# Kernel tuning notes

Hardware: AMD Instinct MI355X
Metric: run time of the kernel (lower is better)

## Reference

```python
import jax, jax.numpy as jnp
import numpy as np

B, S, HID = 1, 2048, 4096
H, NOPE, ROPE, VD = 32, 128, 64, 128
QKD = NOPE + ROPE
Q_RANK, KV_RANK = 1536, 512
IDX_H, IDX_D, TOPK = 16, 128, 1024
EPS, THETA = 1e-5, 10000.0


def rmsnorm(x, w):
    return x * jax.lax.rsqrt(jnp.mean(x * x, axis=-1, keepdims=True) + EPS) * w


def rope_interleaved(x, pos):
    # x: [..., s, d]; rope_interleave=True -> rotate adjacent pairs
    d = x.shape[-1]
    inv_freq = 1.0 / (THETA ** (jnp.arange(0, d, 2, dtype=jnp.float32) / d))
    ang = pos[:, None] * inv_freq[None, :]  # [s, d/2]
    cos, sin = jnp.cos(ang), jnp.sin(ang)
    x2 = x.reshape(*x.shape[:-1], d // 2, 2)
    x0, x1 = x2[..., 0], x2[..., 1]
    return jnp.stack([x0 * cos - x1 * sin, x1 * cos + x0 * sin], axis=-1).reshape(x.shape)


def setup_inputs() -> dict:
    key = jax.random.key(0)
    ks = jax.random.split(key, 12)
    s = 0.02
    return {
        'hidden_states': jax.random.normal(ks[0], (B, S, HID), jnp.float32),
        'q_a_w': jax.random.normal(ks[1], (HID, Q_RANK), jnp.float32) * s,
        'q_a_norm_w': jnp.ones((Q_RANK,), jnp.float32),
        'q_b_w': jax.random.normal(ks[2], (Q_RANK, H * QKD), jnp.float32) * s,
        'kv_a_w': jax.random.normal(ks[3], (HID, KV_RANK + ROPE), jnp.float32) * s,
        'kv_a_norm_w': jnp.ones((KV_RANK,), jnp.float32),
        'kv_b_w': jax.random.normal(ks[4], (KV_RANK, H * (NOPE + VD)), jnp.float32) * s,
        'o_w': jax.random.normal(ks[5], (H * VD, HID), jnp.float32) * s,
        'idx_wq_w': jax.random.normal(ks[6], (HID, IDX_H * IDX_D), jnp.float32) * s,
        'idx_wk_w': jax.random.normal(ks[7], (HID, IDX_D), jnp.float32) * s,
        'idx_weights_w': jax.random.normal(ks[8], (HID, IDX_H), jnp.float32) * s,
    }


def reference(hidden_states, q_a_w, q_a_norm_w, q_b_w, kv_a_w, kv_a_norm_w,
              kv_b_w, o_w, idx_wq_w, idx_wk_w, idx_weights_w):
    b, s, _ = hidden_states.shape
    pos = jnp.arange(s, dtype=jnp.float32)

    # ---- MLA latent projections ----
    q_lat = rmsnorm(hidden_states @ q_a_w, q_a_norm_w)                 # [b,s,Q_RANK]
    q = (q_lat @ q_b_w).reshape(b, s, H, QKD).transpose(0, 2, 1, 3)    # [b,h,s,qkd]
    q_nope, q_pe = q[..., :NOPE], q[..., NOPE:]

    ckv = hidden_states @ kv_a_w                                       # [b,s,KV_RANK+ROPE]
    kv_lat, k_pe = ckv[..., :KV_RANK], ckv[..., KV_RANK:]
    kv = (rmsnorm(kv_lat, kv_a_norm_w) @ kv_b_w).reshape(b, s, H, NOPE + VD).transpose(0, 2, 1, 3)
    k_nope, v = kv[..., :NOPE], kv[..., NOPE:]

    q_pe = rope_interleaved(q_pe, pos)
    k_pe = rope_interleaved(k_pe[:, None, :, :], pos)                  # [b,1,s,ROPE] shared MQA rope head

    scores = (jnp.einsum('bhqd,bhkd->bhqk', q_nope, k_nope)
              + jnp.einsum('bhqd,bhkd->bhqk', q_pe, k_pe)) * (QKD ** -0.5)

    # ---- DSA lightning indexer: per-query top-k key selection ----
    iq = (hidden_states @ idx_wq_w).reshape(b, s, IDX_H, IDX_D)
    ik = hidden_states @ idx_wk_w                                      # [b,s,IDX_D]
    iw = (hidden_states @ idx_weights_w) * (IDX_H ** -0.5)             # [b,s,IDX_H]
    idx_scores = jnp.einsum('bqn,bnqk->bqk', iw,
                            jax.nn.relu(jnp.einsum('bqnd,bkd->bnqk', iq, ik))) * (IDX_D ** -0.5)
    causal = pos[:, None] >= pos[None, :]                              # [s,s]
    idx_scores = jnp.where(causal, idx_scores, -jnp.inf)
    _, topk_idx = jax.lax.top_k(idx_scores, TOPK)                      # [b,s,TOPK]
    bi = jnp.arange(b)[:, None, None]
    qi = jnp.arange(s)[None, :, None]
    topk_mask = jnp.zeros((b, s, s), bool).at[bi, qi, topk_idx].set(True)
    mask = topk_mask & causal                                          # [b,s,s]

    scores = jnp.where(mask[:, None], scores, -jnp.inf)
    attn = jax.nn.softmax(scores, axis=-1)
    out = jnp.einsum('bhqk,bhkd->bqhd', attn, v).reshape(b, s, H * VD)
    return out @ o_w
```

## Files before the change

### kernel.cpp

```cpp
#include <hip/hip_runtime.h>
#include <math.h>

#define S_LEN 2048
#define HIDDEN 4096
#define NHEAD 32
#define D_NOPE 128
#define D_ROPE 64
#define D_V 128
#define D_QK 192
#define QRANK 1536
#define KVRANK 512
#define IDXH 16
#define IDXD 128
#define KSEL 1024
#define NIDX 2304

typedef __attribute__((ext_vector_type(8))) short bf16x8;
typedef __attribute__((ext_vector_type(4))) float f32x4;
typedef __attribute__((ext_vector_type(4))) unsigned short u16x4;

__device__ __forceinline__ unsigned short f2b(float f) {
    union { float f; unsigned int u; } x; x.f = f;
    unsigned int r = x.u + 0x7FFFu + ((x.u >> 16) & 1u);
    return (unsigned short)(r >> 16);
}
__device__ __forceinline__ float b2f(unsigned short u) {
    union { unsigned int u; float f; } x; x.u = ((unsigned int)u) << 16; return x.f;
}

__device__ __forceinline__ void gload16(const void* g, const void* l) {
    __builtin_amdgcn_global_load_lds(
        (const __attribute__((address_space(1))) unsigned int*)(unsigned long long)g,
        (__attribute__((address_space(3))) unsigned int*)(unsigned int)(unsigned long long)l,
        16, 0, 0);
}

template <int OUT_BF16>
__global__ __launch_bounds__(256) void gemm_bf16(const unsigned short* __restrict__ A,
                                                 const unsigned short* __restrict__ Bt,
                                                 void* __restrict__ Cv,
                                                 int K, int ldc, float alpha) {
    __shared__ __align__(16) unsigned char lds[32768];
    const int tid = threadIdx.x;
    const int w = tid >> 6, lane = tid & 63;
    const int lr = lane & 15, g = lane >> 4;
    const int gx = gridDim.x;
    const int nwg = gx * gridDim.y;
    const int flat = blockIdx.y * gx + blockIdx.x;
    const int swz = (flat & 7) * (nwg >> 3) + (flat >> 3);
    const int bm = (swz / gx) * 128, bn = (swz % gx) * 128;
    const int wm = (w >> 1) * 64, wn = (w & 1) * 64;

    f32x4 acc[4][4];
#pragma unroll
    for (int i = 0; i < 4; ++i)
#pragma unroll
        for (int j = 0; j < 4; ++j) acc[i][j] = (f32x4){0.f, 0.f, 0.f, 0.f};

    int a_off[2], b_off[2];
#pragma unroll
    for (int issue = 0; issue < 2; ++issue) {
        const int off = issue * 4096 + w * 1024 + lane * 16;
        const int row = off >> 6, slot = (off >> 4) & 3;
        a_off[issue] = (bm + row) * K + ((slot ^ (row & 3)) << 3);
        b_off[issue] = (bn + row) * K + ((slot ^ (row & 3)) << 3);
    }

    const int KT = K >> 5;
    auto stage = [&](int t, int buf) {
        const int k0 = t << 5;
        unsigned char* l = lds + buf * 16384;
        gload16(A + a_off[0] + k0, l + w * 1024);
        gload16(A + a_off[1] + k0, l + 4096 + w * 1024);
        gload16(Bt + b_off[0] + k0, l + 8192 + w * 1024);
        gload16(Bt + b_off[1] + k0, l + 8192 + 4096 + w * 1024);
    };

    stage(0, 0);
    for (int t = 0; t < KT; ++t) {
        if (t + 1 < KT) {
            stage(t + 1, (t + 1) & 1);
            asm volatile("s_waitcnt vmcnt(4)" ::: "memory");
        } else {
            asm volatile("s_waitcnt vmcnt(0)" ::: "memory");
        }
        __syncthreads();
        const unsigned char* l = lds + (t & 1) * 16384;

        bf16x8 af[4], bfr[4];
#pragma unroll
        for (int i = 0; i < 4; ++i) {
            const int rowA = wm + i * 16 + lr;
            af[i] = *(const bf16x8*)(l + rowA * 64 + ((g ^ (rowA & 3)) << 4));
            const int rowB = wn + i * 16 + lr;
            bfr[i] = *(const bf16x8*)(l + 8192 + rowB * 64 + ((g ^ (rowB & 3)) << 4));
        }
#pragma unroll
        for (int i = 0; i < 4; ++i)
#pragma unroll
            for (int j = 0; j < 4; ++j)
                acc[i][j] = __builtin_amdgcn_mfma_f32_16x16x32_bf16(af[i], bfr[j], acc[i][j], 0, 0, 0);
        __syncthreads();
    }

#pragma unroll
    for (int i = 0; i < 4; ++i) {
        const int m = bm + wm + i * 16 + g * 4;
#pragma unroll
        for (int j = 0; j < 4; ++j) {
            const int n = bn + wn + j * 16 + lr;
            if (OUT_BF16) {
                unsigned short* Cb = (unsigned short*)Cv;
#pragma unroll
                for (int r = 0; r < 4; ++r)
                    Cb[(size_t)(m + r) * ldc + n] = f2b(acc[i][j][r] * alpha);
            } else {
                float* Cf = (float*)Cv;
#pragma unroll
                for (int r = 0; r < 4; ++r)
                    Cf[(size_t)(m + r) * ldc + n] = acc[i][j][r] * alpha;
            }
        }
    }
}

__global__ __launch_bounds__(256) void gemm_split(const unsigned short* __restrict__ Ah,
                                                  const unsigned short* __restrict__ Al,
                                                  const unsigned short* __restrict__ Bh,
                                                  const unsigned short* __restrict__ Bl,
                                                  float* __restrict__ C0,
                                                  float* __restrict__ C1) {
    const int K = HIDDEN, ldc = NIDX;
    const int bid = blockIdx.x;
    const int wf = (bid & 7) * 38 + (bid >> 3);
    const int kz = (wf >= 152) ? 1 : 0;
    const int wgid = wf - kz * 152;
    int x, y;
    if (wgid < 144) { y = 8 + wgid / 18; x = wgid % 18; }
    else            { x = 16; y = wgid - 144; }
    const int bm = y * 128, bn = x * 128;
    float* __restrict__ C = kz ? C1 : C0;

    __shared__ __align__(16) unsigned char lds[65536];
    const int tid = threadIdx.x;
    const int w = tid >> 6, lane = tid & 63;
    const int lr = lane & 15, g = lane >> 4;
    const int wm = (w >> 1) * 64, wn = (w & 1) * 64;

    f32x4 acc[4][4];
#pragma unroll
    for (int i = 0; i < 4; ++i)
#pragma unroll
        for (int j = 0; j < 4; ++j) acc[i][j] = (f32x4){0.f, 0.f, 0.f, 0.f};

    int a_off[2], b_off[2];
#pragma unroll
    for (int issue = 0; issue < 2; ++issue) {
        const int off = issue * 4096 + w * 1024 + lane * 16;
        const int row = off >> 6, slot = (off >> 4) & 3;
        a_off[issue] = (bm + row) * K + ((slot ^ (row & 3)) << 3) + kz * 2048;
        b_off[issue] = (bn + row) * K + ((slot ^ (row & 3)) << 3) + kz * 2048;
    }

    const int KT = 2048 >> 5;
    auto stage = [&](int t, int buf) {
        const int k0 = t << 5;
        unsigned char* l = lds + buf * 32768;
        gload16(Ah + a_off[0] + k0, l + w * 1024);
        gload16(Ah + a_off[1] + k0, l + 4096 + w * 1024);
        gload16(Al + a_off[0] + k0, l + 8192 + w * 1024);
        gload16(Al + a_off[1] + k0, l + 8192 + 4096 + w * 1024);
        gload16(Bh + b_off[0] + k0, l + 16384 + w * 1024);
        gload16(Bh + b_off[1] + k0, l + 16384 + 4096 + w * 1024);
        gload16(Bl + b_off[0] + k0, l + 24576 + w * 1024);
        gload16(Bl + b_off[1] + k0, l + 24576 + 4096 + w * 1024);
    };

    stage(0, 0);
    for (int t = 0; t < KT; ++t) {
        if (t + 1 < KT) {
            stage(t + 1, (t + 1) & 1);
            asm volatile("s_waitcnt vmcnt(8)" ::: "memory");
        } else {
            asm volatile("s_waitcnt vmcnt(0)" ::: "memory");
        }
        __syncthreads();
        const unsigned char* l = lds + (t & 1) * 32768;

        bf16x8 afh[4], afl[4], bfh[4], bfl[4];
#pragma unroll
        for (int i = 0; i < 4; ++i) {
            const int rowA = wm + i * 16 + lr;
            const int offA = rowA * 64 + ((g ^ (rowA & 3)) << 4);
            afh[i] = *(const bf16x8*)(l + offA);
            afl[i] = *(const bf16x8*)(l + 8192 + offA);
            const int rowB = wn + i * 16 + lr;
            const int offB = rowB * 64 + ((g ^ (rowB & 3)) << 4);
            bfh[i] = *(const bf16x8*)(l + 16384 + offB);
            bfl[i] = *(const bf16x8*)(l + 24576 + offB);
        }
#pragma unroll
        for (int i = 0; i < 4; ++i)
#pragma unroll
            for (int j = 0; j < 4; ++j) {
                acc[i][j] = __builtin_amdgcn_mfma_f32_16x16x32_bf16(afh[i], bfh[j], acc[i][j], 0, 0, 0);
                acc[i][j] = __builtin_amdgcn_mfma_f32_16x16x32_bf16(afh[i], bfl[j], acc[i][j], 0, 0, 0);
                acc[i][j] = __builtin_amdgcn_mfma_f32_16x16x32_bf16(afl[i], bfh[j], acc[i][j], 0, 0, 0);
            }
        __syncthreads();
    }

#pragma unroll
    for (int i = 0; i < 4; ++i) {
        const int m = bm + wm + i * 16 + g * 4;
#pragma unroll
        for (int j = 0; j < 4; ++j) {
            const int n = bn + wn + j * 16 + lr;
#pragma unroll
            for (int r = 0; r < 4; ++r)
                C[(size_t)(m + r) * ldc + n] = acc[i][j][r];
        }
    }
}

__global__ __launch_bounds__(256) void conv_split_h(const float* __restrict__ src,
                                                    unsigned short* __restrict__ dhi,
                                                    unsigned short* __restrict__ dlo) {
    const int i = blockIdx.x * 256 + threadIdx.x;
    const float4 v = ((const float4*)src)[i];
    u16x4 hi, lo;
    const float xs[4] = {v.x, v.y, v.z, v.w};
#pragma unroll
    for (int j = 0; j < 4; ++j) {
        const unsigned short h = f2b(xs[j]);
        hi[j] = h;
        lo[j] = f2b(xs[j] - b2f(h));
    }
    *(u16x4*)(dhi + (size_t)i * 4) = hi;
    *(u16x4*)(dlo + (size_t)i * 4) = lo;
}

__global__ __launch_bounds__(256) void conv_split_iq(const float* __restrict__ C0,
                                                     const float* __restrict__ C1,
                                                     unsigned short* __restrict__ iqh,
                                                     unsigned short* __restrict__ iql,
                                                     unsigned short* __restrict__ ikh,
                                                     unsigned short* __restrict__ ikl,
                                                     float* __restrict__ iwbuf) {
    const int i = blockIdx.x * 256 + threadIdx.x;
    const int row = i / 548, c4 = (i - row * 548) * 4;
    const float4 v0 = *(const float4*)(C0 + (size_t)row * NIDX + c4);
    const float4 v1 = *(const float4*)(C1 + (size_t)row * NIDX + c4);
    const float xs[4] = {v0.x + v1.x, v0.y + v1.y, v0.z + v1.z, v0.w + v1.w};
    if (c4 >= 2176) {
        *(float4*)(iwbuf + (size_t)row * 16 + (c4 - 2176)) =
            (float4){xs[0], xs[1], xs[2], xs[3]};
        return;
    }
    u16x4 hi, lo;
#pragma unroll
    for (int j = 0; j < 4; ++j) {
        const unsigned short h = f2b(xs[j]);
        hi[j] = h;
        lo[j] = f2b(xs[j] - b2f(h));
    }
    if (c4 < 2048) {
        *(u16x4*)(iqh + (size_t)row * 2048 + c4) = hi;
        *(u16x4*)(iql + (size_t)row * 2048 + c4) = lo;
    } else {
        *(u16x4*)(ikh + (size_t)row * 128 + c4 - 2048) = hi;
        *(u16x4*)(ikl + (size_t)row * 128 + c4 - 2048) = lo;
    }
}

__global__ __launch_bounds__(256) void wtrans(const float* __restrict__ W,
                                              unsigned short* __restrict__ Bt,
                                              int K, int Nsrc) {
    const int n0 = blockIdx.x * 64, k0 = blockIdx.y * 64;
    __shared__ unsigned short lv[64][72];
    const int tid = threadIdx.x;
#pragma unroll
    for (int it = 0; it < 16; ++it) {
        const int idx = tid + it * 256;
        const int kr = idx >> 6, n = idx & 63;
        const float v = (n0 + n < Nsrc) ? W[(size_t)(k0 + kr) * Nsrc + n0 + n] : 0.f;
        lv[n][kr] = f2b(v);
    }
    __syncthreads();
#pragma unroll
    for (int it = 0; it < 16; ++it) {
        const int idx = tid + it * 256;
        const int n = idx >> 6, kk = idx & 63;
        Bt[(size_t)(n0 + n) * K + k0 + kk] = lv[n][kk];
    }
}

__global__ __launch_bounds__(256) void wtrans_split(const float* __restrict__ W,
                                                    unsigned short* __restrict__ Bth,
                                                    unsigned short* __restrict__ Btl,
                                                    int K, int Nsrc) {
    const int n0 = blockIdx.x * 64, k0 = blockIdx.y * 64;
    __shared__ float lv[64][65];
    const int tid = threadIdx.x;
#pragma unroll
    for (int it = 0; it < 16; ++it) {
        const int idx = tid + it * 256;
        const int kr = idx >> 6, n = idx & 63;
        lv[n][kr] = (n0 + n < Nsrc) ? W[(size_t)(k0 + kr) * Nsrc + n0 + n] : 0.f;
    }
    __syncthreads();
#pragma unroll
    for (int it = 0; it < 16; ++it) {
        const int idx = tid + it * 256;
        const int n = idx >> 6, kk = idx & 63;
        const float x = lv[n][kk];
        const unsigned short h = f2b(x);
        Bth[(size_t)(n0 + n) * K + k0 + kk] = h;
        Btl[(size_t)(n0 + n) * K + k0 + kk] = f2b(x - b2f(h));
    }
}

__global__ __launch_bounds__(256) void rmsnormb(const float* __restrict__ in,
                                                const float* __restrict__ w,
                                                unsigned short* __restrict__ out,
                                                int W, int in_stride) {
    const int row = blockIdx.x;
    const int tid = threadIdx.x;
    const float* x = in + (size_t)row * in_stride;
    float ss = 0.f;
    for (int i = tid; i < W; i += 256) {
        float v = x[i];
        ss += v * v;
    }
    __shared__ float red[256];
    red[tid] = ss;
    __syncthreads();
    for (int s = 128; s > 0; s >>= 1) {
        if (tid < s) red[tid] += red[tid + s];
        __syncthreads();
    }
    const float scale = rsqrtf(red[0] / (float)W + 1e-5f);
    for (int i = tid; i < W; i += 256) out[(size_t)row * W + i] = f2b(x[i] * scale * w[i]);
}

__global__ __launch_bounds__(256) void rope_q16(unsigned short* __restrict__ q) {
    const int idx = blockIdx.x * 256 + threadIdx.x;
    if (idx >= S_LEN * NHEAD * (D_ROPE / 2)) return;
    const int i = idx & 31;
    const int h = (idx >> 5) & 31;
    const int s = idx >> 10;
    const float inv = __expf(-(float)i * (logf(10000.f) / 32.f));
    const float ang = (float)s * inv;
    const float cs = cosf(ang), sn = sinf(ang);
    unsigned short* p = q + (size_t)s * (NHEAD * D_QK) + h * D_QK + D_NOPE + 2 * i;
    const float x0 = b2f(p[0]), x1 = b2f(p[1]);
    p[0] = f2b(x0 * cs - x1 * sn);
    p[1] = f2b(x1 * cs + x0 * sn);
}

__global__ __launch_bounds__(256) void rope_k16(const float* __restrict__ C1,
                                                unsigned short* __restrict__ kpe16) {
    const int idx = blockIdx.x * 256 + threadIdx.x;
    if (idx >= S_LEN * (D_ROPE / 2)) return;
    const int i = idx & 31;
    const int s = idx >> 5;
    const float inv = __expf(-(float)i * (logf(10000.f) / 32.f));
    const float ang = (float)s * inv;
    const float cs = cosf(ang), sn = sinf(ang);
    const float* p = C1 + (size_t)s * 2176 + 2048 + 2 * i;
    const float x0 = p[0], x1 = p[1];
    kpe16[(size_t)s * D_ROPE + 2 * i] = f2b(x0 * cs - x1 * sn);
    kpe16[(size_t)s * D_ROPE + 2 * i + 1] = f2b(x1 * cs + x0 * sn);
}

#define ISC_IKH 0
#define ISC_IKL 16384
#define ISC_IQH 32768
#define ISC_IQL 49152
#define ISC_IW 65536

__global__ __launch_bounds__(256) void idx_score_mfma(const unsigned short* __restrict__ iqh,
                                                      const unsigned short* __restrict__ iql,
                                                      const unsigned short* __restrict__ ikh,
                                                      const unsigned short* __restrict__ ikl,
                                                      const float* __restrict__ iwbuf,
                                                      float* __restrict__ iscore) {
    const int kt = blockIdx.x, qt = blockIdx.y + 16;
    if (kt > qt) return;
    const int q0 = qt * 64, k0 = kt * 64;
    __shared__ __align__(16) unsigned char smem[69632];
    const int tid = threadIdx.x;
    const int w = tid >> 6, lane = tid & 63;
    const int g = lane >> 4, lr = lane & 15;

#pragma unroll
    for (int it = 0; it < 4; ++it) {
        const int j = tid + it * 256;
        const int row = j >> 4, slot = j & 15;
        const int dst = row * 256 + ((slot ^ (row & 7)) << 4);
        *(uint4*)(smem + ISC_IKH + dst) = *(const uint4*)(ikh + (size_t)(k0 + row) * 128 + slot * 8);
        *(uint4*)(smem + ISC_IKL + dst) = *(const uint4*)(ikl + (size_t)(k0 + row) * 128 + slot * 8);
    }
    {
        const int r = tid >> 2, c4 = (tid & 3) * 4;
        const float4 v = *(const float4*)(iwbuf + (size_t)(q0 + r) * 16 + c4);
        float4 sv = {v.x * 0.25f, v.y * 0.25f, v.z * 0.25f, v.w * 0.25f};
        *(float4*)(smem + ISC_IW + r * 64 + c4 * 4) = sv;
    }

    f32x4 tot[4];
#pragma unroll
    for (int j = 0; j < 4; ++j) tot[j] = (f32x4){0.f, 0.f, 0.f, 0.f};

    for (int n = 0; n < IDXH; ++n) {
        __syncthreads();
#pragma unroll
        for (int it = 0; it < 4; ++it) {
            const int j = tid + it * 256;
            const int row = j >> 4, slot = j & 15;
            const int dst = row * 256 + ((slot ^ (row & 7)) << 4);
            *(uint4*)(smem + ISC_IQH + dst) =
                *(const uint4*)(iqh + (size_t)(q0 + row) * 2048 + n * 128 + slot * 8);
            *(uint4*)(smem + ISC_IQL + dst) =
                *(const uint4*)(iql + (size_t)(q0 + row) * 2048 + n * 128 + slot * 8);
        }
        __syncthreads();

        bf16x8 aH[4], aL[4];
        const int ar = w * 16 + lr;
#pragma unroll
        for (int kk = 0; kk < 4; ++kk) {
            const int off = ar * 256 + (((kk * 4 + g) ^ (ar & 7)) << 4);
            aH[kk] = *(const bf16x8*)(smem + ISC_IQH + off);
            aL[kk] = *(const bf16x8*)(smem + ISC_IQL + off);
        }
        float wv[4];
#pragma unroll
        for (int r = 0; r < 4; ++r)
            wv[r] = *(const float*)(smem + ISC_IW + (w * 16 + g * 4 + r) * 64 + n * 4);

#pragma unroll
        for (int jj = 0; jj < 4; ++jj) {
            f32x4 s = (f32x4){0.f, 0.f, 0.f, 0.f};
#pragma unroll
            for (int kk = 0; kk < 4; ++kk) {
                const int br = jj * 16 + lr;
                const int off = br * 256 + (((kk * 4 + g) ^ (br & 7)) << 4);
                const bf16x8 bH = *(const bf16x8*)(smem + ISC_IKH + off);
                const bf16x8 bL = *(const bf16x8*)(smem + ISC_IKL + off);
                s = __builtin_amdgcn_mfma_f32_16x16x32_bf16(aH[kk], bH, s, 0, 0, 0);
                s = __builtin_amdgcn_mfma_f32_16x16x32_bf16(aH[kk], bL, s, 0, 0, 0);
                s = __builtin_amdgcn_mfma_f32_16x16x32_bf16(aL[kk], bH, s, 0, 0, 0);
            }
#pragma unroll
            for (int r = 0; r < 4; ++r) tot[jj][r] += wv[r] * fmaxf(s[r], 0.f);
        }
    }

    const float sc = 0.08838834764831845f;
#pragma unroll
    for (int jj = 0; jj < 4; ++jj)
#pragma unroll
        for (int r = 0; r < 4; ++r)
            iscore[(size_t)(q0 + w * 16 + g * 4 + r) * S_LEN + k0 + jj * 16 + lr] =
                tot[jj][r] * sc;
}

__global__ __launch_bounds__(256) void topk_kernel(const float* __restrict__ iscore,
                                                   unsigned char* __restrict__ maskb) {
    const int q = blockIdx.x;
    const int tid = threadIdx.x;
    const int nk = q + 1;
    unsigned char* mrow = maskb + (size_t)q * 256;
    if (nk <= KSEL) {
        unsigned char b = 0;
#pragma unroll
        for (int bi = 0; bi < 8; ++bi)
            if (tid * 8 + bi <= q) b |= (unsigned char)(1 << bi);
        mrow[tid] = b;
        return;
    }
    __shared__ unsigned int uv[S_LEN];
    __shared__ unsigned int hist[256];
    __shared__ unsigned int sh_pfx, sh_rem;
    const float* srow = iscore + (size_t)q * S_LEN;
    for (int k = tid; k < nk; k += 256) {
        unsigned int b = __float_as_uint(srow[k]);
        uv[k] = (b & 0x80000000u) ? ~b : (b | 0x80000000u);
    }
    if (tid == 0) { sh_pfx = 0u; sh_rem = KSEL; }
    __syncthreads();

    const int lane = tid & 63;
#pragma unroll
    for (int shift = 24; shift >= 0; shift -= 8) {
        const unsigned int pfx = sh_pfx;
        const unsigned int rem = sh_rem;
        const unsigned int pmask = (shift == 24) ? 0u : (0xFFFFFFFFu << (shift + 8));
        hist[tid] = 0u;
        __syncthreads();
        for (int k = tid; k < nk; k += 256) {
            const unsigned int u = uv[k];
            if ((u & pmask) == pfx)
                atomicAdd(&hist[(u >> shift) & 255u], 1u);
        }
        __syncthreads();
        const unsigned int h0 = hist[lane * 4], h1 = hist[lane * 4 + 1];
        const unsigned int h2 = hist[lane * 4 + 2], h3 = hist[lane * 4 + 3];
        unsigned int sufp = h0 + h1 + h2 + h3;
#pragma unroll
        for (int off = 1; off < 64; off <<= 1) {
            const unsigned int o = __shfl_down(sufp, off);
            if (lane + off < 64) sufp += o;
        }
        unsigned int run = __shfl_down(sufp, 1);
        if (lane == 63) run = 0u;
        const unsigned int s3 = run + h3;
        const unsigned int s2 = s3 + h2;
        const unsigned int s1 = s2 + h1;
        const unsigned int s0 = s1 + h0;
        int bsel = -1;
        unsigned int gt = 0u;
        if (s3 >= rem && run < rem)      { bsel = 3; gt = run; }
        else if (s2 >= rem && s3 < rem)  { bsel = 2; gt = s3; }
        else if (s1 >= rem && s2 < rem)  { bsel = 1; gt = s2; }
        else if (s0 >= rem && s1 < rem)  { bsel = 0; gt = s1; }
        if (bsel >= 0) {
            sh_pfx = pfx | ((unsigned int)(lane * 4 + bsel) << shift);
            sh_rem = rem - gt;
        }
        __syncthreads();
    }
    const unsigned int T = sh_pfx;
    const int r = (int)sh_rem;
    unsigned char b = 0;
#pragma unroll
    for (int bi = 0; bi < 8; ++bi) {
        const int k = tid * 8 + bi;
        if (k < nk) {
            const unsigned int u = uv[k];
            if (u > T) {
                b |= (unsigned char)(1 << bi);
            } else if (u == T) {
                int rank = 0;
                for (int j = 0; j < k; ++j) rank += (uv[j] == T) ? 1 : 0;
                if (rank < r) b |= (unsigned char)(1 << bi);
            }
        }
    }
    mrow[tid] = b;
}

__global__ __launch_bounds__(256) void pack_k16(const unsigned short* __restrict__ kv16,
                                                const unsigned short* __restrict__ kpe16,
                                                unsigned short* __restrict__ kb16) {
    const int idx = blockIdx.x * 256 + threadIdx.x;
    const int h = idx / (S_LEN * D_QK);
    const int rem = idx - h * (S_LEN * D_QK);
    const int s = rem / D_QK;
    const int d = rem - s * D_QK;
    kb16[idx] = (d < 128) ? kv16[(size_t)s * 8192 + h * 256 + d]
                          : kpe16[(size_t)s * D_ROPE + (d - 128)];
}

__global__ __launch_bounds__(256) void pack_vT16(const unsigned short* __restrict__ kv16,
                                                 unsigned short* __restrict__ vT) {
    const int st = blockIdx.x, h = blockIdx.y;
    const int s0 = st * 64;
    __shared__ unsigned short lv[64][130];
    const int tid = threadIdx.x;
#pragma unroll
    for (int it = 0; it < 32; ++it) {
        const int idx = tid + it * 256;
        const int sl = idx >> 7, d = idx & 127;
        lv[sl][d] = kv16[(size_t)(s0 + sl) * 8192 + h * 256 + 128 + d];
    }
    __syncthreads();
#pragma unroll
    for (int it = 0; it < 32; ++it) {
        const int idx = tid + it * 256;
        const int d = idx >> 6, sl = idx & 63;
        vT[(size_t)(h * 128 + d) * S_LEN + s0 + sl] = lv[sl][d];
    }
}

#define KVB 64
#define AQB 128
#define AT_K0 0
#define AT_K1 24576
#define AT_V0 49152
#define AT_V1 65536
#define AT_P 81920
#define AT_M 100352
#define AT_TOT 133120

__global__ __launch_bounds__(512) void attn_mfma_kernel(
    const unsigned short* __restrict__ qbuf16,
    const unsigned short* __restrict__ kb16,
    const unsigned short* __restrict__ vT,
    const unsigned char* __restrict__ maskb,
    unsigned short* __restrict__ ab16) {
    __shared__ __align__(16) unsigned char smem[AT_TOT];
    const int bid = blockIdx.x;
    const int xcd = bid & 7, jj = bid >> 3;
    const int h = (xcd << 2) | (jj & 3);
    const int qt = 15 - (jj >> 2);
    const int q0 = qt * AQB;
    const int tid = threadIdx.x;
    const int w = tid >> 6, lane = tid & 63;
    const int g = lane >> 4, lr = lane & 15;
    const int wub = (tid & ~63) * 16;

    const unsigned char* kbase = (const unsigned char*)(kb16 + (size_t)h * S_LEN * D_QK);
    const unsigned char* vbase = (const unsigned char*)(vT + (size_t)h * 128 * S_LEN);
    const unsigned char* mbase = maskb + (size_t)q0 * 256;

    bf16x8 qf[6];
    {
        const unsigned short* qrow =
            qbuf16 + (size_t)(q0 + w * 16 + lr) * (NHEAD * D_QK) + h * D_QK;
#pragma unroll
        for (int c = 0; c < 6; ++c) qf[c] = *(const bf16x8*)(qrow + c * 32 + g * 8);
    }

#pragma unroll
    for (int it = 0; it < 4; ++it) {
        const int j = tid + it * 512;
        gload16(mbase + (size_t)j * 16, smem + AT_M + it * 8192 + wub);
    }

    auto stageK = [&](int k0, int kb) {
#pragma unroll
        for (int it = 0; it < 3; ++it) {
            const int j = tid + it * 512;
            const int row = j / 24, cs = j - row * 24;
            const int scs = (cs & ~7) | ((cs & 7) ^ (row & 7));
            gload16(kbase + (size_t)(k0 + row) * 384 + scs * 16, smem + kb + it * 8192 + wub);
        }
    };
    auto stageV = [&](int k0, int vb) {
#pragma unroll
        for (int it = 0; it < 2; ++it) {
            const int j = tid + it * 512;
            const int d = j >> 3, sl = j & 7;
            gload16(vbase + ((size_t)d * S_LEN + k0) * 2 + ((sl ^ (d & 7)) * 16),
                    smem + vb + it * 8192 + wub);
        }
    };

    f32x4 O[8];
#pragma unroll
    for (int db = 0; db < 8; ++db) O[db] = (f32x4){0.f, 0.f, 0.f, 0.f};
    float mS[4] = {-INFINITY, -INFINITY, -INFINITY, -INFINITY};
    float lS[4] = {0.f, 0.f, 0.f, 0.f};
    unsigned short* Pw = (unsigned short*)(smem + AT_P + w * 2304);

    const int nt = 2 * qt + 2;
    stageK(0, AT_K0);
    stageV(0, AT_V0);
    asm volatile("s_waitcnt vmcnt(0)" ::: "memory");
    __syncthreads();

    for (int t = 0; t < nt; ++t) {
        const int cK = AT_K0 + (t & 1) * 24576;
        const int cV = AT_V0 + (t & 1) * 16384;
        if (t + 1 < nt) {
            stageK((t + 1) * KVB, AT_K0 + ((t + 1) & 1) * 24576);
            stageV((t + 1) * KVB, AT_V0 + ((t + 1) & 1) * 16384);
        }

        f32x4 a[4];
#pragma unroll
        for (int j = 0; j < 4; ++j) a[j] = (f32x4){0.f, 0.f, 0.f, 0.f};
        __builtin_amdgcn_s_setprio(1);
#pragma unroll
        for (int c = 0; c < 6; ++c) {
            const int s = c * 4 + g;
#pragma unroll
            for (int j = 0; j < 4; ++j) {
                const int row = j * 16 + lr;
                const int scs = (s & ~7) | ((s & 7) ^ (lr & 7));
                const bf16x8 b = *(const bf16x8*)(smem + cK + row * 384 + scs * 16);
                a[j] = __builtin_amdgcn_mfma_f32_16x16x32_bf16(qf[c], b, a[j], 0, 0, 0);
            }
        }
        __builtin_amdgcn_s_setprio(0);

        const int moff = (t * KVB) >> 3;
        float corr[4];
#pragma unroll
        for (int r = 0; r < 4; ++r) {
            const int qrl = w * 16 + g * 4 + r;
            const unsigned int mlo = *(const unsigned int*)(smem + AT_M + qrl * 256 + moff);
            const unsigned int mhi = *(const unsigned int*)(smem + AT_M + qrl * 256 + moff + 4);
            float sv[4];
            sv[0] = ((mlo >> lr) & 1u) ? a[0][r] : -INFINITY;
            sv[1] = ((mlo >> (lr + 16)) & 1u) ? a[1][r] : -INFINITY;
            sv[2] = ((mhi >> lr) & 1u) ? a[2][r] : -INFINITY;
            sv[3] = ((mhi >> (lr + 16)) & 1u) ? a[3][r] : -INFINITY;
            float tm = fmaxf(fmaxf(sv[0], sv[1]), fmaxf(sv[2], sv[3]));
            tm = fmaxf(tm, __shfl_xor(tm, 1));
            tm = fmaxf(tm, __shfl_xor(tm, 2));
            tm = fmaxf(tm, __shfl_xor(tm, 4));
            tm = fmaxf(tm, __shfl_xor(tm, 8));
            const float mn = fmaxf(mS[r], tm);
            const float co = (mS[r] > -INFINITY) ? __expf(mS[r] - mn) : 0.f;
            float p[4];
#pragma unroll
            for (int j = 0; j < 4; ++j) p[j] = (sv[j] > -INFINITY) ? __expf(sv[j] - mn) : 0.f;
            float rs = (p[0] + p[1]) + (p[2] + p[3]);
            rs += __shfl_xor(rs, 1);
            rs += __shfl_xor(rs, 2);
            rs += __shfl_xor(rs, 4);
            rs += __shfl_xor(rs, 8);
            lS[r] = lS[r] * co + rs;
            mS[r] = mn;
            corr[r] = co;
#pragma unroll
            for (int j = 0; j < 4; ++j) Pw[(g * 4 + r) * 72 + j * 16 + lr] = f2b(p[j]);
        }
#pragma unroll
        for (int db = 0; db < 8; ++db) {
            O[db][0] *= corr[0];
            O[db][1] *= corr[1];
            O[db][2] *= corr[2];
            O[db][3] *= corr[3];
        }

        asm volatile("s_waitcnt lgkmcnt(0)" ::: "memory");
        __builtin_amdgcn_sched_barrier(0);

        __builtin_amdgcn_s_setprio(1);
#pragma unroll
        for (int c2 = 0; c2 < 2; ++c2) {
            const bf16x8 pA = *(const bf16x8*)((const unsigned char*)Pw + lr * 144 + c2 * 64 + g * 16);
#pragma unroll
            for (int db = 0; db < 8; ++db) {
                const int d = db * 16 + lr;
                const int s2 = c2 * 4 + g;
                const bf16x8 bV = *(const bf16x8*)(smem + cV + d * 128 + ((s2 ^ (d & 7)) << 4));
                O[db] = __builtin_amdgcn_mfma_f32_16x16x32_bf16(pA, bV, O[db], 0, 0, 0);
            }
        }
        __builtin_amdgcn_s_setprio(0);

        asm volatile("s_waitcnt vmcnt(0)" ::: "memory");
        __syncthreads();
    }

#pragma unroll
    for (int r = 0; r < 4; ++r) {
        const float inv = (lS[r] > 0.f) ? 1.f / lS[r] : 0.f;
        const int qg = q0 + w * 16 + g * 4 + r;
        unsigned short* orow = ab16 + (size_t)qg * (NHEAD * D_V) + h * D_V;
#pragma unroll
        for (int db = 0; db < 8; ++db) orow[db * 16 + lr] = f2b(O[db][r] * inv);
    }
}

extern "C" void kernel_launch(void* const* d_in, const int* in_sizes, int n_in,
                              void* d_out, int out_size, void* d_ws, size_t ws_size,
                              hipStream_t stream) {
    const float* hidden        = (const float*)d_in[0];
    const float* q_a_w         = (const float*)d_in[1];
    const float* q_a_norm_w    = (const float*)d_in[2];
    const float* q_b_w         = (const float*)d_in[3];
    const float* kv_a_w        = (const float*)d_in[4];
    const float* kv_a_norm_w   = (const float*)d_in[5];
    const float* kv_b_w        = (const float*)d_in[6];
    const float* o_w           = (const float*)d_in[7];
    const float* idx_wq_w      = (const float*)d_in[8];
    const float* idx_wk_w      = (const float*)d_in[9];
    const float* idx_weights_w = (const float*)d_in[10];
    float* out = (float*)d_out;

    char* ws = (char*)d_ws;
    unsigned short* BtAll = (unsigned short*)(ws + 0);
    unsigned short* kv16  = (unsigned short*)(ws + 0);
    unsigned short* owT   = (unsigned short*)(ws + 0);
    unsigned short* h16    = (unsigned short*)(ws + 33554432);
    unsigned short* h_lo   = (unsigned short*)(ws + 50331648);
    unsigned short* qbuf16 = (unsigned short*)(ws + 33554432);
    float* C1          = (float*)(ws + 67108864);
    unsigned short* vT = (unsigned short*)(ws + 67108864);
    unsigned short* BtIdxH = (unsigned short*)(ws + 84934656);
    unsigned short* BtIdxL = (unsigned short*)(ws + 103809024);
    unsigned short* kb16   = (unsigned short*)(ws + 84934656);
    float* Cidx         = (float*)(ws + 122683392);
    unsigned short* qbT = (unsigned short*)(ws + 122683392);
    unsigned short* iqh  = (unsigned short*)(ws + 141557760);
    unsigned short* iql  = (unsigned short*)(ws + 149946368);
    unsigned short* ikh  = (unsigned short*)(ws + 158334976);
    unsigned short* ikl  = (unsigned short*)(ws + 158859264);
    unsigned short* kvbT = (unsigned short*)(ws + 141557760);
    float* iscr          = (float*)(ws + 159383552);
    unsigned short* ab16 = (unsigned short*)(ws + 159383552);
    unsigned char* maskb  = (unsigned char*)(ws + 176160768);
    unsigned short* qa16  = (unsigned short*)(ws + 180355072);
    unsigned short* kvn16 = (unsigned short*)(ws + 186646528);
    unsigned short* kpe16 = (unsigned short*)(ws + 188743680);
    float* iwbuf = (float*)(ws + 189005824);
    float* Cidx2 = (float*)(ws + 189136896);
    (void)ws_size; (void)in_sizes; (void)n_in; (void)out_size;

    const dim3 blk(256);
    const float QK_SCALE = 0.07216878364870323f;

    conv_split_h<<<8192, blk, 0, stream>>>(hidden, h16, h_lo);

    wtrans<<<dim3(24, 64), blk, 0, stream>>>(q_a_w, BtAll, HIDDEN, QRANK);
    wtrans<<<dim3(9, 64), blk, 0, stream>>>(kv_a_w, BtAll + (size_t)1536 * HIDDEN, HIDDEN, KVRANK + D_ROPE);
    wtrans<<<dim3(1, 64), blk, 0, stream>>>(q_a_w, BtAll + (size_t)2112 * HIDDEN, HIDDEN, 0);
    gemm_bf16<0><<<dim3(17, 16), blk, 0, stream>>>(h16, BtAll, C1, HIDDEN, 2176, 1.f);

    rmsnormb<<<S_LEN, blk, 0, stream>>>(C1, q_a_norm_w, qa16, QRANK, 2176);
    rmsnormb<<<S_LEN, blk, 0, stream>>>(C1 + 1536, kv_a_norm_w, kvn16, KVRANK, 2176);
    rope_k16<<<(S_LEN * 32 + 255) / 256, blk, 0, stream>>>(C1, kpe16);

    wtrans_split<<<dim3(32, 64), blk, 0, stream>>>(idx_wq_w, BtIdxH, BtIdxL, HIDDEN, IDXH * IDXD);
    wtrans_split<<<dim3(2, 64), blk, 0, stream>>>(idx_wk_w, BtIdxH + (size_t)2048 * HIDDEN,
                                                  BtIdxL + (size_t)2048 * HIDDEN, HIDDEN, IDXD);
    wtrans_split<<<dim3(2, 64), blk, 0, stream>>>(idx_weights_w, BtIdxH + (size_t)2176 * HIDDEN,
                                                  BtIdxL + (size_t)2176 * HIDDEN, HIDDEN, IDXH);
    gemm_split<<<dim3(304), blk, 0, stream>>>(h16, h_lo, BtIdxH, BtIdxL, Cidx, Cidx2);
    conv_split_iq<<<4384, blk, 0, stream>>>(Cidx, Cidx2, iqh, iql, ikh, ikl, iwbuf);
    idx_score_mfma<<<dim3(32, 16), blk, 0, stream>>>(iqh, iql, ikh, ikl, iwbuf, iscr);
    topk_kernel<<<S_LEN, blk, 0, stream>>>(iscr, maskb);

    wtrans<<<dim3(96, 24), blk, 0, stream>>>(q_b_w, qbT, QRANK, NHEAD * D_QK);
    wtrans<<<dim3(128, 8), blk, 0, stream>>>(kv_b_w, kvbT, KVRANK, NHEAD * 256);
    gemm_bf16<1><<<dim3(48, 16), blk, 0, stream>>>(qa16, qbT, qbuf16, QRANK, NHEAD * D_QK, QK_SCALE);
    gemm_bf16<1><<<dim3(64, 16), blk, 0, stream>>>(kvn16, kvbT, kv16, KVRANK, NHEAD * 256, 1.f);
    rope_q16<<<(S_LEN * NHEAD * 32 + 255) / 256, blk, 0, stream>>>(qbuf16);

    pack_k16<<<(NHEAD * S_LEN * D_QK) / 256, blk, 0, stream>>>(kv16, kpe16, kb16);
    pack_vT16<<<dim3(S_LEN / 64, NHEAD), blk, 0, stream>>>(kv16, vT);
    attn_mfma_kernel<<<dim3(512), dim3(512), 0, stream>>>(qbuf16, kb16, vT, maskb, ab16);

    wtrans<<<dim3(64, 64), blk, 0, stream>>>(o_w, owT, NHEAD * D_V, HIDDEN);
    gemm_bf16<0><<<dim3(32, 16), blk, 0, stream>>>(ab16, owT, out, NHEAD * D_V, HIDDEN, 1.f);
}
```

Measured before the change: 773.0 us.

## Fuse kv_b GEMM epilogue into K/V^T packing and slim attention LDS usage

Adds a dedicated kv_b GEMM whose epilogue writes the K-nope part directly into the per-head packed K buffer and transposes V tiles through LDS straight into vT. Rope for k_pe is broadcast straight into each head's slot of the packed K buffer. This removes the intermediate kv16/kpe16 buffers and the pack_k16/pack_vT16 kernels. The attention kernel now loads mask bits into registers per tile instead of staging the whole mask in LDS, and reuses the current K buffer for P behind an extra barrier. Together these shrink LDS from about 130KB to 80KB, and O rescaling is skipped when the correction factor is exactly 1. The costs are an added barrier per tile, more scattered global mask reads and strided K stores from the GEMM epilogue.

```diff
diff --git a/kernel.cpp b/kernel.cpp
--- a/kernel.cpp
+++ b/kernel.cpp
@@ -121,6 +121,109 @@
                     Cf[(size_t)(m + r) * ldc + n] = acc[i][j][r] * alpha;
             }
         }
+    }
+}
+
+__global__ __launch_bounds__(256) void gemm_kvb(const unsigned short* __restrict__ A,
+                                                const unsigned short* __restrict__ Bt,
+                                                unsigned short* __restrict__ kb16,
+                                                unsigned short* __restrict__ vT) {
+    __shared__ __align__(16) unsigned char lds[34816];
+    const int tid = threadIdx.x;
+    const int w = tid >> 6, lane = tid & 63;
+    const int lr = lane & 15, g = lane >> 4;
+    const int gx = gridDim.x;
+    const int nwg = gx * gridDim.y;
+    const int flat = blockIdx.y * gx + blockIdx.x;
+    const int swz = (flat & 7) * (nwg >> 3) + (flat >> 3);
+    const int bm = (swz / gx) * 128, bn = (swz % gx) * 128;
+    const int wm = (w >> 1) * 64, wn = (w & 1) * 64;
+    const int K = KVRANK;
+
+    f32x4 acc[4][4];
+#pragma unroll
+    for (int i = 0; i < 4; ++i)
+#pragma unroll
+        for (int j = 0; j < 4; ++j) acc[i][j] = (f32x4){0.f, 0.f, 0.f, 0.f};
+
+    int a_off[2], b_off[2];
+#pragma unroll
+    for (int issue = 0; issue < 2; ++issue) {
+        const int off = issue * 4096 + w * 1024 + lane * 16;
+        const int row = off >> 6, slot = (off >> 4) & 3;
+        a_off[issue] = (bm + row) * K + ((slot ^ (row & 3)) << 3);
+        b_off[issue] = (bn + row) * K + ((slot ^ (row & 3)) << 3);
+    }
+
+    const int KT = K >> 5;
+    auto stage = [&](int t, int buf) {
+        const int k0 = t << 5;
+        unsigned char* l = lds + buf * 16384;
+        gload16(A + a_off[0] + k0, l + w * 1024);
+        gload16(A + a_off[1] + k0, l + 4096 + w * 1024);
+        gload16(Bt + b_off[0] + k0, l + 8192 + w * 1024);
+        gload16(Bt + b_off[1] + k0, l + 8192 + 4096 + w * 1024);
+    };
+
+    stage(0, 0);
+    for (int t = 0; t < KT; ++t) {
+        if (t + 1 < KT) {
+            stage(t + 1, (t + 1) & 1);
+            asm volatile("s_waitcnt vmcnt(4)" ::: "memory");
+        } else {
+            asm volatile("s_waitcnt vmcnt(0)" ::: "memory");
+        }
+        __syncthreads();
+        const unsigned char* l = lds + (t & 1) * 16384;
+
+        bf16x8 af[4], bfr[4];
+#pragma unroll
+        for (int i = 0; i < 4; ++i) {
+            const int rowA = wm + i * 16 + lr;
+            af[i] = *(const bf16x8*)(l + rowA * 64 + ((g ^ (rowA & 3)) << 4));
+            const int rowB = wn + i * 16 + lr;
+            bfr[i] = *(const bf16x8*)(l + 8192 + rowB * 64 + ((g ^ (rowB & 3)) << 4));
+        }
+#pragma unroll
+        for (int i = 0; i < 4; ++i)
+#pragma unroll
+            for (int j = 0; j < 4; ++j)
+                acc[i][j] = __builtin_amdgcn_mfma_f32_16x16x32_bf16(af[i], bfr[j], acc[i][j], 0, 0, 0);
+        __syncthreads();
+    }
+
+    const int h = bn >> 8;
+    if ((bn & 128) == 0) {
+#pragma unroll
+        for (int i = 0; i < 4; ++i) {
+            const int m = bm + wm + i * 16 + g * 4;
+#pragma unroll
+            for (int j = 0; j < 4; ++j) {
+                const int dl = wn + j * 16 + lr;
+#pragma unroll
+                for (int r = 0; r < 4; ++r)
+                    kb16[((size_t)h * S_LEN + m + r) * D_QK + dl] = f2b(acc[i][j][r]);
+            }
+        }
+    } else {
+        unsigned short(*T)[136] = (unsigned short(*)[136])lds;
+#pragma unroll
+        for (int i = 0; i < 4; ++i) {
+            const int ml = wm + i * 16 + g * 4;
+#pragma unroll
+            for (int j = 0; j < 4; ++j) {
+                const int dl = wn + j * 16 + lr;
+#pragma unroll
+                for (int r = 0; r < 4; ++r) T[dl][ml + r] = f2b(acc[i][j][r]);
+            }
+        }
+        __syncthreads();
+        const int row = tid >> 1, half = tid & 1;
+        unsigned short* dst = vT + (size_t)(h * 128 + row) * S_LEN + bm + half * 64;
+        const unsigned short* src = &T[row][half * 64];
+#pragma unroll
+        for (int u = 0; u < 8; ++u)
+            *(uint4*)(dst + u * 8) = *(const uint4*)(src + u * 8);
     }
 }
 
@@ -358,19 +461,20 @@
     p[1] = f2b(x1 * cs + x0 * sn);
 }
 
-__global__ __launch_bounds__(256) void rope_k16(const float* __restrict__ C1,
-                                                unsigned short* __restrict__ kpe16) {
+__global__ __launch_bounds__(256) void rope_k16b(const float* __restrict__ C1,
+                                                 unsigned short* __restrict__ kb16) {
     const int idx = blockIdx.x * 256 + threadIdx.x;
-    if (idx >= S_LEN * (D_ROPE / 2)) return;
     const int i = idx & 31;
-    const int s = idx >> 5;
+    const int s = (idx >> 5) & 2047;
+    const int h = idx >> 16;
     const float inv = __expf(-(float)i * (logf(10000.f) / 32.f));
     const float ang = (float)s * inv;
     const float cs = cosf(ang), sn = sinf(ang);
     const float* p = C1 + (size_t)s * 2176 + 2048 + 2 * i;
     const float x0 = p[0], x1 = p[1];
-    kpe16[(size_t)s * D_ROPE + 2 * i] = f2b(x0 * cs - x1 * sn);
-    kpe16[(size_t)s * D_ROPE + 2 * i + 1] = f2b(x1 * cs + x0 * sn);
+    unsigned short* o = kb16 + ((size_t)h * S_LEN + s) * D_QK + D_NOPE + 2 * i;
+    o[0] = f2b(x0 * cs - x1 * sn);
+    o[1] = f2b(x1 * cs + x0 * sn);
 }
 
 #define ISC_IKH 0
@@ -551,48 +655,11 @@
     mrow[tid] = b;
 }
 
-__global__ __launch_bounds__(256) void pack_k16(const unsigned short* __restrict__ kv16,
-                                                const unsigned short* __restrict__ kpe16,
-                                                unsigned short* __restrict__ kb16) {
-    const int idx = blockIdx.x * 256 + threadIdx.x;
-    const int h = idx / (S_LEN * D_QK);
-    const int rem = idx - h * (S_LEN * D_QK);
-    const int s = rem / D_QK;
-    const int d = rem - s * D_QK;
-    kb16[idx] = (d < 128) ? kv16[(size_t)s * 8192 + h * 256 + d]
-                          : kpe16[(size_t)s * D_ROPE + (d - 128)];
-}
-
-__global__ __launch_bounds__(256) void pack_vT16(const unsigned short* __restrict__ kv16,
-                                                 unsigned short* __restrict__ vT) {
-    const int st = blockIdx.x, h = blockIdx.y;
-    const int s0 = st * 64;
-    __shared__ unsigned short lv[64][130];
-    const int tid = threadIdx.x;
-#pragma unroll
-    for (int it = 0; it < 32; ++it) {
-        const int idx = tid + it * 256;
-        const int sl = idx >> 7, d = idx & 127;
-        lv[sl][d] = kv16[(size_t)(s0 + sl) * 8192 + h * 256 + 128 + d];
-    }
-    __syncthreads();
-#pragma unroll
-    for (int it = 0; it < 32; ++it) {
-        const int idx = tid + it * 256;
-        const int d = idx >> 6, sl = idx & 63;
-        vT[(size_t)(h * 128 + d) * S_LEN + s0 + sl] = lv[sl][d];
-    }
-}
-
 #define KVB 64
 #define AQB 128
 #define AT_K0 0
-#define AT_K1 24576
 #define AT_V0 49152
-#define AT_V1 65536
-#define AT_P 81920
-#define AT_M 100352
-#define AT_TOT 133120
+#define AT_TOT 81920
 
 __global__ __launch_bounds__(512) void attn_mfma_kernel(
     const unsigned short* __restrict__ qbuf16,
@@ -623,12 +690,6 @@
         for (int c = 0; c < 6; ++c) qf[c] = *(const bf16x8*)(qrow + c * 32 + g * 8);
     }
 
-#pragma unroll
-    for (int it = 0; it < 4; ++it) {
-        const int j = tid + it * 512;
-        gload16(mbase + (size_t)j * 16, smem + AT_M + it * 8192 + wub);
-    }
-
     auto stageK = [&](int k0, int kb) {
 #pragma unroll
         for (int it = 0; it < 3; ++it) {
@@ -653,7 +714,6 @@
     for (int db = 0; db < 8; ++db) O[db] = (f32x4){0.f, 0.f, 0.f, 0.f};
     float mS[4] = {-INFINITY, -INFINITY, -INFINITY, -INFINITY};
     float lS[4] = {0.f, 0.f, 0.f, 0.f};
-    unsigned short* Pw = (unsigned short*)(smem + AT_P + w * 2304);
 
     const int nt = 2 * qt + 2;
     stageK(0, AT_K0);
@@ -664,9 +724,13 @@
     for (int t = 0; t < nt; ++t) {
         const int cK = AT_K0 + (t & 1) * 24576;
         const int cV = AT_V0 + (t & 1) * 16384;
+        uint2 mreg[4];
+#pragma unroll
+        for (int r = 0; r < 4; ++r)
+            mreg[r] = *(const uint2*)(mbase + (size_t)(w * 16 + g * 4 + r) * 256 + t * 8);
         if (t + 1 < nt) {
-            stageK((t + 1) * KVB, AT_K0 + ((t + 1) & 1) * 24576);
-            stageV((t + 1) * KVB, AT_V0 + ((t + 1) & 1) * 16384);
+            stageK((t + 1) * KVB, AT_K0 + (((t + 1) & 1)) * 24576);
+            stageV((t + 1) * KVB, AT_V0 + (((t + 1) & 1)) * 16384);
         }
 
         f32x4 a[4];
@@ -686,13 +750,15 @@
         }
         __builtin_amdgcn_s_setprio(0);
 
-        const int moff = (t * KVB) >> 3;
+        __builtin_amdgcn_sched_barrier(0);
+        asm volatile("s_barrier" ::: "memory");
+        __builtin_amdgcn_sched_barrier(0);
+        unsigned short* Pw = (unsigned short*)(smem + cK + w * 2304);
+
         float corr[4];
 #pragma unroll
         for (int r = 0; r < 4; ++r) {
-            const int qrl = w * 16 + g * 4 + r;
-            const unsigned int mlo = *(const unsigned int*)(smem + AT_M + qrl * 256 + moff);
-            const unsigned int mhi = *(const unsigned int*)(smem + AT_M + qrl * 256 + moff + 4);
+            const unsigned int mlo = mreg[r].x, mhi = mreg[r].y;
             float sv[4];
             sv[0] = ((mlo >> lr) & 1u) ? a[0][r] : -INFINITY;
             sv[1] = ((mlo >> (lr + 16)) & 1u) ? a[1][r] : -INFINITY;
@@ -720,11 +786,11 @@
             for (int j = 0; j < 4; ++j) Pw[(g * 4 + r) * 72 + j * 16 + lr] = f2b(p[j]);
         }
 #pragma unroll
-        for (int db = 0; db < 8; ++db) {
-            O[db][0] *= corr[0];
-            O[db][1] *= corr[1];
-            O[db][2] *= corr[2];
-            O[db][3] *= corr[3];
+        for (int r = 0; r < 4; ++r) {
+            if (corr[r] != 1.0f) {
+#pragma unroll
+                for (int db = 0; db < 8; ++db) O[db][r] *= corr[r];
+            }
         }
 
         asm volatile("s_waitcnt lgkmcnt(0)" ::: "memory");
@@ -776,7 +842,6 @@
 
     char* ws = (char*)d_ws;
     unsigned short* BtAll = (unsigned short*)(ws + 0);
-    unsigned short* kv16  = (unsigned short*)(ws + 0);
     unsigned short* owT   = (unsigned short*)(ws + 0);
     unsigned short* h16    = (unsigned short*)(ws + 33554432);
     unsigned short* h_lo   = (unsigned short*)(ws + 50331648);
@@ -798,7 +863,6 @@
     unsigned char* maskb  = (unsigned char*)(ws + 176160768);
     unsigned short* qa16  = (unsigned short*)(ws + 180355072);
     unsigned short* kvn16 = (unsigned short*)(ws + 186646528);
-    unsigned short* kpe16 = (unsigned short*)(ws + 188743680);
     float* iwbuf = (float*)(ws + 189005824);
     float* Cidx2 = (float*)(ws + 189136896);
     (void)ws_size; (void)in_sizes; (void)n_in; (void)out_size;
@@ -815,7 +879,6 @@
 
     rmsnormb<<<S_LEN, blk, 0, stream>>>(C1, q_a_norm_w, qa16, QRANK, 2176);
     rmsnormb<<<S_LEN, blk, 0, stream>>>(C1 + 1536, kv_a_norm_w, kvn16, KVRANK, 2176);
-    rope_k16<<<(S_LEN * 32 + 255) / 256, blk, 0, stream>>>(C1, kpe16);
 
     wtrans_split<<<dim3(32, 64), blk, 0, stream>>>(idx_wq_w, BtIdxH, BtIdxL, HIDDEN, IDXH * IDXD);
     wtrans_split<<<dim3(2, 64), blk, 0, stream>>>(idx_wk_w, BtIdxH + (size_t)2048 * HIDDEN,
@@ -827,14 +890,14 @@
     idx_score_mfma<<<dim3(32, 16), blk, 0, stream>>>(iqh, iql, ikh, ikl, iwbuf, iscr);
     topk_kernel<<<S_LEN, blk, 0, stream>>>(iscr, maskb);
 
+    rope_k16b<<<(NHEAD * S_LEN * 32) / 256, blk, 0, stream>>>(C1, kb16);
+
     wtrans<<<dim3(96, 24), blk, 0, stream>>>(q_b_w, qbT, QRANK, NHEAD * D_QK);
     wtrans<<<dim3(128, 8), blk, 0, stream>>>(kv_b_w, kvbT, KVRANK, NHEAD * 256);
     gemm_bf16<1><<<dim3(48, 16), blk, 0, stream>>>(qa16, qbT, qbuf16, QRANK, NHEAD * D_QK, QK_SCALE);
-    gemm_bf16<1><<<dim3(64, 16), blk, 0, stream>>>(kvn16, kvbT, kv16, KVRANK, NHEAD * 256, 1.f);
+    gemm_kvb<<<dim3(64, 16), blk, 0, stream>>>(kvn16, kvbT, kb16, vT);
     rope_q16<<<(S_LEN * NHEAD * 32 + 255) / 256, blk, 0, stream>>>(qbuf16);
 
-    pack_k16<<<(NHEAD * S_LEN * D_QK) / 256, blk, 0, stream>>>(kv16, kpe16, kb16);
-    pack_vT16<<<dim3(S_LEN / 64, NHEAD), blk, 0, stream>>>(kv16, vT);
     attn_mfma_kernel<<<dim3(512), dim3(512), 0, stream>>>(qbuf16, kb16, vT, maskb, ab16);
 
     wtrans<<<dim3(64, 64), blk, 0, stream>>>(o_w, owT, NHEAD * D_V, HIDDEN);
```

Measured after the change: 768.8 us. About the same (-0.6%).
